# Kernel tuning notes

Measured on AMD Instinct MI355X. Metric: run time of the kernel, lower is better.

Reference implementation:

```python
import jax, jax.numpy as jnp
import numpy as np

B, S, H, E, V, OOV = 64, 400, 512, 256, 50000, 100

def setup_inputs() -> dict:
    key = jax.random.key(0)
    ks = jax.random.split(key, 32)
    p = lambda i, shape: jax.random.normal(ks[i], shape, jnp.float32) * 0.02
    emb = p(0, (V, E)).at[0].set(0.0)  # padding_idx=0
    return dict(
        summaries_in=jax.random.randint(ks[1], (B,), 1, V),
        h0=jax.random.normal(ks[2], (B, H), jnp.float32),
        c0=jax.random.normal(ks[3], (B, H), jnp.float32),
        encoder_out=jax.random.normal(ks[4], (B, S, 2 * H), jnp.float32),
        encoder_features=jax.random.normal(ks[5], (S * B, 2 * H), jnp.float32),
        encoder_mask=jnp.ones((S, B), jnp.float32),
        context=jax.random.normal(ks[6], (B, 2 * H), jnp.float32),
        coverage=jax.random.uniform(ks[7], (S, B), jnp.float32) * 0.01,
        texts_extended=jax.random.randint(ks[8], (S, B), 0, V + OOV),
        oov_size=OOV,
        emb=emb,
        W_feat=p(10, (2 * H, 2 * H)), b_feat=p(11, (2 * H,)),
        W_cov=p(12, (2 * H,)), b_cov=p(13, (2 * H,)),
        w_att=p(14, (2 * H,)), b_att=p(15, ()),
        W_ih=p(16, (4 * H, E)), W_hh=p(17, (4 * H, H)),
        b_ih=p(18, (4 * H,)), b_hh=p(19, (4 * H,)),
        W_ctx=p(20, (E, 2 * H + E)), b_ctx=p(21, (E,)),
        W_pg=p(22, (4 * H + E,)), b_pg=p(23, ()),
        W_o1=p(24, (H, 3 * H)), b_o1=p(25, (H,)),
        W_o2=p(26, (V, H)), b_o2=p(27, (V,)),
    )


def reference(summaries_in, h0, c0, encoder_out, encoder_features, encoder_mask,
              context, coverage, texts_extended, oov_size, emb,
              W_feat, b_feat, W_cov, b_cov, w_att, b_att,
              W_ih, W_hh, b_ih, b_hh, W_ctx, b_ctx, W_pg, b_pg,
              W_o1, b_o1, W_o2, b_o2):
    # embedding + context projection: [B, 2H+E] -> [B, E]
    x = emb[summaries_in]
    ctx_out = jnp.concatenate([context, x], axis=1) @ W_ctx.T + b_ctx
    # single LSTM step (torch gate order i, f, g, o)
    gates = ctx_out @ W_ih.T + b_ih + h0 @ W_hh.T + b_hh
    i, f, g, o = jnp.split(gates, 4, axis=1)
    c = jax.nn.sigmoid(f) * c0 + jax.nn.sigmoid(i) * jnp.tanh(g)
    h = jax.nn.sigmoid(o) * jnp.tanh(c)
    hidden_out = jnp.concatenate([h, c], axis=1)  # [B, 2H]
    # Bahdanau attention with coverage
    dec_feat = hidden_out @ W_feat.T + b_feat                 # [B, 2H]
    ef = encoder_features.reshape(S, B, 2 * H)                # [S, B, 2H]
    cov_feat = coverage[..., None] * W_cov + b_cov            # Linear(1, 2H)
    e = jnp.tanh(ef + dec_feat[None] + cov_feat) @ w_att + b_att  # [S, B]
    a = jax.nn.softmax(e, axis=0) * encoder_mask
    a = a / jnp.sum(a, axis=0, keepdims=True)                 # renormalize (Normalize(0))
    ctx_new = jnp.einsum('sb,bsd->bd', a, encoder_out)        # [B, 2H]
    coverage_next = coverage + a
    # pointer-generator mix
    gen_in = jnp.concatenate([ctx_new, hidden_out, ctx_out], axis=1)  # [B, 4H+E]
    p_gen = jax.nn.sigmoid(gen_in @ W_pg + b_pg)[:, None]             # [B, 1]
    logits = (jnp.concatenate([h, ctx_new], axis=1) @ W_o1.T + b_o1) @ W_o2.T + b_o2
    vocab_dist = p_gen * jax.nn.softmax(logits, axis=1)       # [B, V]
    attn_w = (1.0 - p_gen) * a.T                              # [B, S]
    vd = jnp.concatenate([vocab_dist, jnp.zeros((B, oov_size), vocab_dist.dtype)], axis=1)
    vd = vd.at[jnp.arange(B)[:, None], texts_extended.T].add(attn_w)  # scatter_add copy dist
    return vd, hidden_out, ctx_new, a, coverage_next
```

## Files before the change

kernel.cpp:

```cpp
#include <hip/hip_runtime.h>
#include <cmath>

#define B 64
#define S 400
#define H 512
#define E 256
#define V 50000
#define OOV 100
#define H2 1024
#define VDN (V + OOV)
#define NBLK_V 782
#define SC 10

typedef __attribute__((ext_vector_type(8))) short short8;
typedef __attribute__((ext_vector_type(4))) float f32x4;

__device__ __forceinline__ float wred_sum(float v) {
#pragma unroll
  for (int o = 32; o > 0; o >>= 1) v += __shfl_down(v, o, 64);
  return v;
}
__device__ __forceinline__ short f2bf(float f) {
  return __builtin_bit_cast(short, (__bf16)f);
}
__device__ __forceinline__ float bf2f(unsigned short u) {
  unsigned x = (unsigned)u << 16;
  return __builtin_bit_cast(float, x);
}
__device__ __forceinline__ float ftanh(float x) {
  float e = __expf(2.f * x);
  return 1.f - 2.f * __builtin_amdgcn_rcpf(e + 1.f);
}
__device__ __forceinline__ float fsig(float x) {
  return __builtin_amdgcn_rcpf(1.f + __expf(-x));
}
__device__ __forceinline__ float wred_max(float v) {
#pragma unroll
  for (int o = 32; o > 0; o >>= 1) v = fmaxf(v, __shfl_down(v, o, 64));
  return v;
}

__global__ __launch_bounds__(256) void k_pre(
    const float* __restrict__ b_ctx, const float* __restrict__ b_ih,
    const float* __restrict__ b_hh, const float* __restrict__ b_feat,
    const float* __restrict__ b_o1, const float* __restrict__ context,
    const float* __restrict__ emb, const int* __restrict__ sumin,
    const float* __restrict__ h0, float* __restrict__ ctxoutT4,
    float* __restrict__ gates, float* __restrict__ dfeat,
    float* __restrict__ innerT4, float* __restrict__ catT4,
    float* __restrict__ h0T4, float* __restrict__ Zb) {
  int idx = blockIdx.x * 256 + threadIdx.x;
  if (idx < 64) Zb[idx] = 0.f;
  if (idx < 16384) {
    int j = ((idx >> 8) << 2) + (idx & 3);
    ctxoutT4[idx] = b_ctx[j];
  } else if (idx < 16384 + 131072) {
    int i = idx - 16384;
    int j = i & 2047;
    gates[i] = b_ih[j] + b_hh[j];
  } else if (idx < 16384 + 131072 + 65536) {
    int i = idx - 16384 - 131072;
    dfeat[i] = b_feat[i & 1023];
  } else if (idx < 245760) {
    int i = idx - 16384 - 131072 - 65536;
    int j = ((i >> 8) << 2) + (i & 3);
    innerT4[i] = b_o1[j];
  } else if (idx < 245760 + 81920) {
    int i = idx - 245760;
    int e = i & 3, b = (i >> 2) & 63, q = i >> 8;
    int k = q * 4 + e;
    catT4[i] = (k < 1024) ? context[b * 1024 + k]
                          : emb[(size_t)sumin[b] * 256 + (k - 1024)];
  } else {
    int i = idx - 245760 - 81920;
    int e = i & 3, b = (i >> 2) & 63, q = i >> 8;
    h0T4[i] = h0[b * 512 + q * 4 + e];
  }
}

template <int R, int KC, int OUTMODE>
__global__ __launch_bounds__(256) void k_gemmsk(
    const float* __restrict__ A1, const float* __restrict__ W1, int ldw1, int s1,
    const float* __restrict__ A2, const float* __restrict__ W2, int ldw2,
    float* __restrict__ out, int ldout) {
  const int lane = threadIdx.x;
  const int w = threadIdx.y;
  const int j0 = blockIdx.x * (4 * R) + w * R;
  const float* A;
  const float* W;
  int ldw, kc0;
  if ((int)blockIdx.y < s1) {
    A = A1; W = W1; ldw = ldw1; kc0 = blockIdx.y * KC;
  } else {
    A = A2; W = W2; ldw = ldw2; kc0 = (blockIdx.y - s1) * KC;
  }
  float acc[R];
#pragma unroll
  for (int r = 0; r < R; ++r) acc[r] = 0.f;
  const float* ap = A + (size_t)kc0 * 256 + lane * 4;
  const float* wr[R];
#pragma unroll
  for (int r = 0; r < R; ++r) wr[r] = W + (size_t)(j0 + r) * ldw + kc0 * 4;
#pragma unroll 8
  for (int k4 = 0; k4 < KC; ++k4) {
    float4 av = *(const float4*)(ap + (size_t)k4 * 256);
#pragma unroll
    for (int r = 0; r < R; ++r) {
      float4 wv = *(const float4*)(wr[r] + k4 * 4);
      acc[r] += av.x * wv.x + av.y * wv.y + av.z * wv.z + av.w * wv.w;
    }
  }
#pragma unroll
  for (int r = 0; r < R; ++r) {
    int j = j0 + r;
    if constexpr (OUTMODE == 0)
      atomicAdd(&out[((size_t)(j >> 2) * 64 + lane) * 4 + (j & 3)], acc[r]);
    else
      atomicAdd(&out[(size_t)lane * ldout + j], acc[r]);
  }
}

__global__ __launch_bounds__(256) void k_lstm(const float* __restrict__ gates,
                                              const float* __restrict__ c0,
                                              float* __restrict__ hidden,
                                              float* __restrict__ hcT4) {
  int idx = blockIdx.x * 256 + threadIdx.x;
  int b = idx >> 9, u = idx & 511;
  float gi = gates[(size_t)b * 2048 + u];
  float gf = gates[(size_t)b * 2048 + 512 + u];
  float gg = gates[(size_t)b * 2048 + 1024 + u];
  float go = gates[(size_t)b * 2048 + 1536 + u];
  float c = fsig(gf) * c0[(size_t)b * 512 + u] + fsig(gi) * ftanh(gg);
  float h = fsig(go) * ftanh(c);
  hidden[(size_t)b * H2 + u] = h;
  hidden[(size_t)b * H2 + 512 + u] = c;
  hcT4[((u >> 2) * 64 + b) * 4 + (u & 3)] = h;
  int k = 512 + u;
  hcT4[((k >> 2) * 64 + b) * 4 + (k & 3)] = c;
}

__global__ __launch_bounds__(256) void k_ectx(
    const float* __restrict__ ef, const float* __restrict__ dfeat,
    const float* __restrict__ cov, const float* __restrict__ Wcov,
    const float* __restrict__ bcov, const float* __restrict__ watt,
    const float* __restrict__ batt, const float* __restrict__ mask,
    const float* __restrict__ enc, float* __restrict__ e_x,
    float* __restrict__ Zb, float* __restrict__ partc) {
  const int t = threadIdx.x;
  const int lane = t & 63;
  const int w = t >> 6;
  const int b = blockIdx.x & 63;
  const int g = blockIdx.x >> 6;
  const int s0 = g * 40 + w * 10;
  float4 dbc[4], wc4[4], wa4[4];
  {
    const float4* dfr = (const float4*)(dfeat + (size_t)b * H2);
    const float4* bcr = (const float4*)bcov;
    const float4* wcr = (const float4*)Wcov;
    const float4* war = (const float4*)watt;
#pragma unroll
    for (int k = 0; k < 4; ++k) {
      int i4 = k * 64 + lane;
      float4 dv = dfr[i4], bc = bcr[i4];
      dbc[k] = make_float4(dv.x + bc.x, dv.y + bc.y, dv.z + bc.z, dv.w + bc.w);
      wc4[k] = wcr[i4];
      wa4[k] = war[i4];
    }
  }
  const float ba = batt[0];
  float4 acc[4];
#pragma unroll
  for (int k = 0; k < 4; ++k) acc[k] = make_float4(0.f, 0.f, 0.f, 0.f);
  float zsum = 0.f;

  for (int i = 0; i < 10; i += 2) {
    const int s1 = s0 + i, s2 = s0 + i + 1;
    const float4* efr1 = (const float4*)(ef + (size_t)(s1 * B + b) * H2);
    const float4* efr2 = (const float4*)(ef + (size_t)(s2 * B + b) * H2);
    const float4* enr1 = (const float4*)(enc + ((size_t)b * S + s1) * H2);
    const float4* enr2 = (const float4*)(enc + ((size_t)b * S + s2) * H2);
    float4 a1[4], a2[4], e1[4], e2[4];
#pragma unroll
    for (int k = 0; k < 4; ++k) {
      int i4 = k * 64 + lane;
      a1[k] = efr1[i4];
      a2[k] = efr2[i4];
      e1[k] = enr1[i4];
      e2[k] = enr2[i4];
    }
    const float c1 = cov[s1 * B + b], c2 = cov[s2 * B + b];
    float d1 = 0.f, d2 = 0.f;
#pragma unroll
    for (int k = 0; k < 4; ++k) {
      d1 += ftanh(a1[k].x + dbc[k].x + c1 * wc4[k].x) * wa4[k].x;
      d1 += ftanh(a1[k].y + dbc[k].y + c1 * wc4[k].y) * wa4[k].y;
      d1 += ftanh(a1[k].z + dbc[k].z + c1 * wc4[k].z) * wa4[k].z;
      d1 += ftanh(a1[k].w + dbc[k].w + c1 * wc4[k].w) * wa4[k].w;
      d2 += ftanh(a2[k].x + dbc[k].x + c2 * wc4[k].x) * wa4[k].x;
      d2 += ftanh(a2[k].y + dbc[k].y + c2 * wc4[k].y) * wa4[k].y;
      d2 += ftanh(a2[k].z + dbc[k].z + c2 * wc4[k].z) * wa4[k].z;
      d2 += ftanh(a2[k].w + dbc[k].w + c2 * wc4[k].w) * wa4[k].w;
    }
#pragma unroll
    for (int o = 32; o > 0; o >>= 1) {
      d1 += __shfl_xor(d1, o, 64);
      d2 += __shfl_xor(d2, o, 64);
    }
    const float x1 = mask[s1 * B + b] * __expf(d1 + ba);
    const float x2 = mask[s2 * B + b] * __expf(d2 + ba);
    if (lane == 0) {
      e_x[s1 * B + b] = x1;
      e_x[s2 * B + b] = x2;
    }
    zsum += x1 + x2;
#pragma unroll
    for (int k = 0; k < 4; ++k) {
      acc[k].x += x1 * e1[k].x + x2 * e2[k].x;
      acc[k].y += x1 * e1[k].y + x2 * e2[k].y;
      acc[k].z += x1 * e1[k].z + x2 * e2[k].z;
      acc[k].w += x1 * e1[k].w + x2 * e2[k].w;
    }
  }
  if (lane == 0) atomicAdd(&Zb[b], zsum);
  __shared__ float4 lacc[4][256];
#pragma unroll
  for (int k = 0; k < 4; ++k) lacc[w][lane * 4 + k] = acc[k];
  __syncthreads();
  if (w == 0) {
#pragma unroll
    for (int k = 0; k < 4; ++k) {
      float4 s = lacc[0][lane * 4 + k];
      float4 s1 = lacc[1][lane * 4 + k];
      float4 s2 = lacc[2][lane * 4 + k];
      float4 s3 = lacc[3][lane * 4 + k];
      s.x += s1.x + s2.x + s3.x;
      s.y += s1.y + s2.y + s3.y;
      s.z += s1.z + s2.z + s3.z;
      s.w += s1.w + s2.w + s3.w;
      ((float4*)(partc + (size_t)blockIdx.x * H2))[k * 64 + lane] = s;
    }
  }
}

__global__ __launch_bounds__(256) void k_ctxpg(
    const float* __restrict__ partc, const float* __restrict__ e_x,
    const float* __restrict__ Zb, const float* __restrict__ coverage,
    const float* __restrict__ hidden, const float* __restrict__ ctxoutT4,
    const float* __restrict__ Wpg, const float* __restrict__ bpg,
    float* __restrict__ ctx_new, float* __restrict__ ctxT4,
    float* __restrict__ pgen, float* __restrict__ a_out,
    float* __restrict__ cov_out) {
  const int b = blockIdx.x;
  const int t = threadIdx.x;
  const int lane = t & 63, w = t >> 6;
  const float rZ = 1.f / Zb[b];
  const int d = t * 4;
  float4 s = make_float4(0.f, 0.f, 0.f, 0.f);
#pragma unroll
  for (int sc = 0; sc < SC; ++sc) {
    float4 v = *(const float4*)(partc + (size_t)(sc * 64 + b) * H2 + d);
    s.x += v.x; s.y += v.y; s.z += v.z; s.w += v.w;
  }
  s.x *= rZ; s.y *= rZ; s.z *= rZ; s.w *= rZ;
  *(float4*)(ctx_new + (size_t)b * H2 + d) = s;
  *(float4*)(ctxT4 + (size_t)t * 256 + b * 4) = s;
#pragma unroll
  for (int i = 0; i < 2; ++i) {
    int sidx = t + i * 256;
    if (sidx < S) {
      int sb = sidx * B + b;
      float av = e_x[sb] * rZ;
      a_out[sb] = av;
      cov_out[sb] = coverage[sb] + av;
    }
  }
  float p = s.x * Wpg[d] + s.y * Wpg[d + 1] + s.z * Wpg[d + 2] + s.w * Wpg[d + 3];
#pragma unroll
  for (int j = 0; j < 4; ++j) {
    int k = t + j * 256;
    p += hidden[(size_t)b * H2 + k] * Wpg[1024 + k];
  }
  p += ctxoutT4[(size_t)(t >> 2) * 256 + b * 4 + (t & 3)] * Wpg[2048 + t];
  p = wred_sum(p);
  __shared__ float red[4];
  if (lane == 0) red[w] = p;
  __syncthreads();
  if (t == 0) {
    float dd = red[0] + red[1] + red[2] + red[3] + bpg[0];
    pgen[b] = fsig(dd);
  }
}

__global__ __launch_bounds__(256) void k_packinner(const float* __restrict__ innerT4,
                                                   short8* __restrict__ packB) {
  int f = blockIdx.x * 256 + threadIdx.x;
  int l = f & 63, bt = (f >> 6) & 3, ks = f >> 8;
  int b = bt * 16 + (l & 15);
  int kbase = ks * 32 + (l >> 4) * 8;
  float4 q0 = *(const float4*)&innerT4[(size_t)(kbase / 4) * 256 + b * 4];
  float4 q1 = *(const float4*)&innerT4[(size_t)(kbase / 4 + 1) * 256 + b * 4];
  short8 frag;
  frag[0] = f2bf(q0.x); frag[1] = f2bf(q0.y);
  frag[2] = f2bf(q0.z); frag[3] = f2bf(q0.w);
  frag[4] = f2bf(q1.x); frag[5] = f2bf(q1.y);
  frag[6] = f2bf(q1.z); frag[7] = f2bf(q1.w);
  packB[f] = frag;
}

__global__ __launch_bounds__(256) void k_mfma_logits(
    const float* __restrict__ W2, const short8* __restrict__ packB,
    const float* __restrict__ bias, unsigned short* __restrict__ logits_bf,
    float* __restrict__ mp, float* __restrict__ zp) {
  const int l = threadIdx.x;
  const int w = threadIdx.y;
  const int jblk = blockIdx.x * 64;
  const int jv = min(jblk + w * 16 + (l & 15), V - 1);
  const float4* wp4 = (const float4*)(W2 + (size_t)jv * 512 + (l >> 4) * 8);

  f32x4 acc0 = {0.f, 0.f, 0.f, 0.f}, acc1 = acc0, acc2 = acc0, acc3 = acc0;
  float4 cw0 = wp4[0], cw1 = wp4[1];
#pragma unroll
  for (int ks = 0; ks < 16; ++ks) {
    float4 nw0, nw1;
    if (ks < 15) { nw0 = wp4[(ks + 1) * 8]; nw1 = wp4[(ks + 1) * 8 + 1]; }
    short8 af;
    af[0] = f2bf(cw0.x); af[1] = f2bf(cw0.y); af[2] = f2bf(cw0.z); af[3] = f2bf(cw0.w);
    af[4] = f2bf(cw1.x); af[5] = f2bf(cw1.y); af[6] = f2bf(cw1.z); af[7] = f2bf(cw1.w);
    short8 b0 = packB[(ks * 4 + 0) * 64 + l];
    short8 b1 = packB[(ks * 4 + 1) * 64 + l];
    short8 b2 = packB[(ks * 4 + 2) * 64 + l];
    short8 b3 = packB[(ks * 4 + 3) * 64 + l];
    acc0 = __builtin_amdgcn_mfma_f32_16x16x32_bf16(af, b0, acc0, 0, 0, 0);
    acc1 = __builtin_amdgcn_mfma_f32_16x16x32_bf16(af, b1, acc1, 0, 0, 0);
    acc2 = __builtin_amdgcn_mfma_f32_16x16x32_bf16(af, b2, acc2, 0, 0, 0);
    acc3 = __builtin_amdgcn_mfma_f32_16x16x32_bf16(af, b3, acc3, 0, 0, 0);
    if (ks < 15) { cw0 = nw0; cw1 = nw1; }
  }

  __shared__ float tile[64][65];
  const int rbase = w * 16 + (l >> 4) * 4;
#pragma unroll
  for (int v = 0; v < 4; ++v) {
    int jl = rbase + v;
    int j = jblk + jl;
    float bv = bias[min(j, V - 1)];
    bool valid = (j < V);
    tile[jl][0 * 16 + (l & 15)] = valid ? acc0[v] + bv : -INFINITY;
    tile[jl][1 * 16 + (l & 15)] = valid ? acc1[v] + bv : -INFINITY;
    tile[jl][2 * 16 + (l & 15)] = valid ? acc2[v] + bv : -INFINITY;
    tile[jl][3 * 16 + (l & 15)] = valid ? acc3[v] + bv : -INFINITY;
  }
  __syncthreads();
  const int t = w * 64 + l;
#pragma unroll
  for (int i = 0; i < 16; ++i) {
    int idx = i * 256 + t;
    int jl = idx & 63;
    int b = idx >> 6;
    int j = jblk + jl;
    if (j < V)
      logits_bf[(size_t)b * V + j] = (unsigned short)f2bf(tile[jl][b]);
  }
  if (t < 64) {
    float m = -INFINITY;
#pragma unroll
    for (int jl = 0; jl < 64; ++jl) m = fmaxf(m, tile[jl][t]);
    float z = 0.f;
#pragma unroll
    for (int jl = 0; jl < 64; ++jl) z += __expf(tile[jl][t] - m);
    mp[(size_t)blockIdx.x * 64 + t] = m;
    zp[(size_t)blockIdx.x * 64 + t] = z;
  }
}

__global__ __launch_bounds__(256) void k_vdms(
    const unsigned short* __restrict__ logits_bf, const float* __restrict__ mp,
    const float* __restrict__ zp, const float* __restrict__ pgen,
    const float* __restrict__ a_out, const int* __restrict__ tex,
    float* __restrict__ out) {
  const int b = blockIdx.x >> 3;
  const int c = blockIdx.x & 7;
  const int t = threadIdx.x;
  const int lane = t & 63, w = t >> 6;
  __shared__ float red[4];
  __shared__ float hist[6272];
  float m = -INFINITY;
  for (int i = t; i < NBLK_V; i += 256) m = fmaxf(m, mp[i * 64 + b]);
  m = wred_max(m);
  if (lane == 0) red[w] = m;
  __syncthreads();
  const float M = fmaxf(fmaxf(red[0], red[1]), fmaxf(red[2], red[3]));
  __syncthreads();
  float z = 0.f;
  for (int i = t; i < NBLK_V; i += 256) z += zp[i * 64 + b] * __expf(mp[i * 64 + b] - M);
  z = wred_sum(z);
  if (lane == 0) red[w] = z;
  __syncthreads();
  const float Z = red[0] + red[1] + red[2] + red[3];
  const float pg = pgen[b];
  const float scale = pg / Z;
  const float wq = 1.f - pg;
  const int v0 = c * 6272;
  const int v1 = min(v0 + 6272, VDN);
  for (int i = t; i < 6272; i += 256) hist[i] = 0.f;
  __syncthreads();
  for (int s = t; s < S; s += 256) {
    int v = tex[s * B + b];
    if (v >= v0 && v < v1) atomicAdd(&hist[v - v0], wq * a_out[s * B + b]);
  }
  __syncthreads();
  for (int v = v0 + t; v < v1; v += 256) {
    float val =
        (v < V) ? scale * __expf(bf2f(logits_bf[(size_t)b * V + v]) - M) : 0.f;
    out[(size_t)b * VDN + v] = val + hist[v - v0];
  }
}

extern "C" void kernel_launch(void* const* d_in, const int* in_sizes, int n_in,
                              void* d_out, int out_size, void* d_ws, size_t ws_size,
                              hipStream_t stream) {
  const int* sumin = (const int*)d_in[0];
  const float* h0 = (const float*)d_in[1];
  const float* c0 = (const float*)d_in[2];
  const float* enc_out = (const float*)d_in[3];
  const float* ef = (const float*)d_in[4];
  const float* mask = (const float*)d_in[5];
  const float* context = (const float*)d_in[6];
  const float* coverage = (const float*)d_in[7];
  const int* tex = (const int*)d_in[8];
  const float* emb = (const float*)d_in[10];
  const float* W_feat = (const float*)d_in[11];
  const float* b_feat = (const float*)d_in[12];
  const float* W_cov = (const float*)d_in[13];
  const float* b_cov = (const float*)d_in[14];
  const float* w_att = (const float*)d_in[15];
  const float* b_att = (const float*)d_in[16];
  const float* W_ih = (const float*)d_in[17];
  const float* W_hh = (const float*)d_in[18];
  const float* b_ih = (const float*)d_in[19];
  const float* b_hh = (const float*)d_in[20];
  const float* W_ctx = (const float*)d_in[21];
  const float* b_ctx = (const float*)d_in[22];
  const float* W_pg = (const float*)d_in[23];
  const float* b_pg = (const float*)d_in[24];
  const float* W_o1 = (const float*)d_in[25];
  const float* b_o1 = (const float*)d_in[26];
  const float* W_o2 = (const float*)d_in[27];
  const float* b_o2 = (const float*)d_in[28];

  float* out = (float*)d_out;
  float* vd = out;
  float* hidden = vd + (size_t)B * VDN;
  float* ctx_new = hidden + (size_t)B * H2;
  float* a_out = ctx_new + (size_t)B * H2;
  float* cov_out = a_out + (size_t)S * B;

  float* ws = (float*)d_ws;
  float* catT4 = ws;
  float* h0T4 = catT4 + 81920;
  float* ctxoutT4 = h0T4 + 32768;
  float* gates = ctxoutT4 + 16384;
  float* hidcatT4 = gates + 131072;
  float* dfeat = hidcatT4 + 65536;
  float* e_x = dfeat + 65536;
  float* ctxnewT4 = e_x + 25600;
  float* innerT4 = ctxnewT4 + 65536;
  float* pgen = innerT4 + 32768;
  float* Zb = pgen + 64;
  float* mp = Zb + 64;
  float* zp = mp + 50048;
  float* packBf = zp + 50048;
  float* logits = packBf + 16384;
  float* partc = logits + 1600064;
  short8* packB = (short8*)packBf;
  unsigned short* logits_bf = (unsigned short*)logits;

  dim3 gblk(64, 4);

  k_pre<<<1408, 256, 0, stream>>>(b_ctx, b_ih, b_hh, b_feat, b_o1, context, emb,
                                  sumin, h0, ctxoutT4, gates, dfeat, innerT4,
                                  catT4, h0T4, Zb);
  k_gemmsk<2, 64, 0><<<dim3(32, 5), gblk, 0, stream>>>(
      catT4, W_ctx, 1280, 5, nullptr, nullptr, 0, ctxoutT4, 0);
  k_gemmsk<2, 64, 1><<<dim3(256, 3), gblk, 0, stream>>>(
      ctxoutT4, W_ih, 256, 1, h0T4, W_hh, 512, gates, 2048);
  k_lstm<<<128, 256, 0, stream>>>(gates, c0, hidden, hidcatT4);
  k_gemmsk<2, 64, 1><<<dim3(128, 4), gblk, 0, stream>>>(
      hidcatT4, W_feat, 1024, 4, nullptr, nullptr, 0, dfeat, 1024);
  k_ectx<<<SC * B, 256, 0, stream>>>(ef, dfeat, coverage, W_cov, b_cov, w_att,
                                     b_att, mask, enc_out, e_x, Zb, partc);
  k_ctxpg<<<B, 256, 0, stream>>>(partc, e_x, Zb, coverage, hidden, ctxoutT4,
                                 W_pg, b_pg, ctx_new, ctxnewT4, pgen, a_out,
                                 cov_out);
  k_gemmsk<2, 64, 0><<<dim3(64, 6), gblk, 0, stream>>>(
      hidcatT4, W_o1, 1536, 2, ctxnewT4, W_o1 + 512, 1536, innerT4, 0);
  k_packinner<<<16, 256, 0, stream>>>(innerT4, packB);
  k_mfma_logits<<<NBLK_V, gblk, 0, stream>>>(W_o2, packB, b_o2, logits_bf, mp, zp);
  k_vdms<<<B * 8, 256, 0, stream>>>(logits_bf, mp, zp, pgen, a_out, tex, vd);
}
```

Baseline: 204.9 us.

## Restructure attention-context kernel for more blocks and upfront loads

The attention energy/context kernel now gives each warp 4 sequence positions instead of 10, so the grid grows from 10 to 25 position groups (SC raised to match). All encoder-feature and encoder-output rows for a warp are loaded into registers up front, behind a scheduling barrier, to expose more memory-level parallelism. Per-batch decoder-feature, coverage and attention weights are staged in shared memory, and the cross-warp reduction of partial contexts is done by all threads. In exchange there is higher register pressure, more partial-context rows for the downstream kernel to reduce, and more atomics on the normaliser.

```diff
diff --git a/kernel.cpp b/kernel.cpp
--- a/kernel.cpp
+++ b/kernel.cpp
@@ -10,7 +10,7 @@
 #define H2 1024
 #define VDN (V + OOV)
 #define NBLK_V 782
-#define SC 10
+#define SC 25
 
 typedef __attribute__((ext_vector_type(8))) short short8;
 typedef __attribute__((ext_vector_type(4))) float f32x4;
@@ -18,6 +18,11 @@
 __device__ __forceinline__ float wred_sum(float v) {
 #pragma unroll
   for (int o = 32; o > 0; o >>= 1) v += __shfl_down(v, o, 64);
+  return v;
+}
+__device__ __forceinline__ float wred_max(float v) {
+#pragma unroll
+  for (int o = 32; o > 0; o >>= 1) v = fmaxf(v, __shfl_down(v, o, 64));
   return v;
 }
 __device__ __forceinline__ short f2bf(float f) {
@@ -33,11 +38,6 @@
 }
 __device__ __forceinline__ float fsig(float x) {
   return __builtin_amdgcn_rcpf(1.f + __expf(-x));
-}
-__device__ __forceinline__ float wred_max(float v) {
-#pragma unroll
-  for (int o = 32; o > 0; o >>= 1) v = fmaxf(v, __shfl_down(v, o, 64));
-  return v;
 }
 
 __global__ __launch_bounds__(256) void k_pre(
@@ -151,94 +151,82 @@
   const int w = t >> 6;
   const int b = blockIdx.x & 63;
   const int g = blockIdx.x >> 6;
-  const int s0 = g * 40 + w * 10;
-  float4 dbc[4], wc4[4], wa4[4];
-  {
-    const float4* dfr = (const float4*)(dfeat + (size_t)b * H2);
-    const float4* bcr = (const float4*)bcov;
-    const float4* wcr = (const float4*)Wcov;
-    const float4* war = (const float4*)watt;
+  const int s0 = g * 16 + w * 4;
+  __shared__ float s_dbc[1024], s_wc[1024], s_wa[1024];
+  for (int i = t; i < 1024; i += 256) {
+    s_dbc[i] = dfeat[(size_t)b * H2 + i] + bcov[i];
+    s_wc[i] = Wcov[i];
+    s_wa[i] = watt[i];
+  }
+  __syncthreads();
+
+  float4 evs[4][4], ens[4][4];
+  float cv[4], mk[4];
+#pragma unroll
+  for (int r = 0; r < 4; ++r) {
+    const int s = s0 + r;
+    const float4* efr = (const float4*)(ef + (size_t)(s * B + b) * H2);
+    const float4* enr = (const float4*)(enc + ((size_t)b * S + s) * H2);
 #pragma unroll
     for (int k = 0; k < 4; ++k) {
-      int i4 = k * 64 + lane;
-      float4 dv = dfr[i4], bc = bcr[i4];
-      dbc[k] = make_float4(dv.x + bc.x, dv.y + bc.y, dv.z + bc.z, dv.w + bc.w);
-      wc4[k] = wcr[i4];
-      wa4[k] = war[i4];
+      evs[r][k] = efr[k * 64 + lane];
+      ens[r][k] = enr[k * 64 + lane];
     }
-  }
+    cv[r] = cov[s * B + b];
+    mk[r] = mask[s * B + b];
+  }
+  __builtin_amdgcn_sched_barrier(0);
+
   const float ba = batt[0];
+  float x[4];
+  float zsum = 0.f;
+#pragma unroll
+  for (int r = 0; r < 4; ++r) {
+    float d = 0.f;
+#pragma unroll
+    for (int k = 0; k < 4; ++k) {
+      const int i4 = (k * 64 + lane) * 4;
+      d += ftanh(evs[r][k].x + s_dbc[i4 + 0] + cv[r] * s_wc[i4 + 0]) * s_wa[i4 + 0];
+      d += ftanh(evs[r][k].y + s_dbc[i4 + 1] + cv[r] * s_wc[i4 + 1]) * s_wa[i4 + 1];
+      d += ftanh(evs[r][k].z + s_dbc[i4 + 2] + cv[r] * s_wc[i4 + 2]) * s_wa[i4 + 2];
+      d += ftanh(evs[r][k].w + s_dbc[i4 + 3] + cv[r] * s_wc[i4 + 3]) * s_wa[i4 + 3];
+    }
+#pragma unroll
+    for (int o = 32; o > 0; o >>= 1) d += __shfl_xor(d, o, 64);
+    x[r] = mk[r] * __expf(d + ba);
+    if (lane == 0) e_x[(s0 + r) * B + b] = x[r];
+    zsum += x[r];
+  }
+  if (lane == 0) atomicAdd(&Zb[b], zsum);
   float4 acc[4];
 #pragma unroll
   for (int k = 0; k < 4; ++k) acc[k] = make_float4(0.f, 0.f, 0.f, 0.f);
-  float zsum = 0.f;
-
-  for (int i = 0; i < 10; i += 2) {
-    const int s1 = s0 + i, s2 = s0 + i + 1;
-    const float4* efr1 = (const float4*)(ef + (size_t)(s1 * B + b) * H2);
-    const float4* efr2 = (const float4*)(ef + (size_t)(s2 * B + b) * H2);
-    const float4* enr1 = (const float4*)(enc + ((size_t)b * S + s1) * H2);
-    const float4* enr2 = (const float4*)(enc + ((size_t)b * S + s2) * H2);
-    float4 a1[4], a2[4], e1[4], e2[4];
+#pragma unroll
+  for (int r = 0; r < 4; ++r) {
 #pragma unroll
     for (int k = 0; k < 4; ++k) {
-      int i4 = k * 64 + lane;
-      a1[k] = efr1[i4];
-      a2[k] = efr2[i4];
-      e1[k] = enr1[i4];
-      e2[k] = enr2[i4];
+      acc[k].x += x[r] * ens[r][k].x;
+      acc[k].y += x[r] * ens[r][k].y;
+      acc[k].z += x[r] * ens[r][k].z;
+      acc[k].w += x[r] * ens[r][k].w;
     }
-    const float c1 = cov[s1 * B + b], c2 = cov[s2 * B + b];
-    float d1 = 0.f, d2 = 0.f;
-#pragma unroll
-    for (int k = 0; k < 4; ++k) {
-      d1 += ftanh(a1[k].x + dbc[k].x + c1 * wc4[k].x) * wa4[k].x;
-      d1 += ftanh(a1[k].y + dbc[k].y + c1 * wc4[k].y) * wa4[k].y;
-      d1 += ftanh(a1[k].z + dbc[k].z + c1 * wc4[k].z) * wa4[k].z;
-      d1 += ftanh(a1[k].w + dbc[k].w + c1 * wc4[k].w) * wa4[k].w;
-      d2 += ftanh(a2[k].x + dbc[k].x + c2 * wc4[k].x) * wa4[k].x;
-      d2 += ftanh(a2[k].y + dbc[k].y + c2 * wc4[k].y) * wa4[k].y;
-      d2 += ftanh(a2[k].z + dbc[k].z + c2 * wc4[k].z) * wa4[k].z;
-      d2 += ftanh(a2[k].w + dbc[k].w + c2 * wc4[k].w) * wa4[k].w;
-    }
-#pragma unroll
-    for (int o = 32; o > 0; o >>= 1) {
-      d1 += __shfl_xor(d1, o, 64);
-      d2 += __shfl_xor(d2, o, 64);
-    }
-    const float x1 = mask[s1 * B + b] * __expf(d1 + ba);
-    const float x2 = mask[s2 * B + b] * __expf(d2 + ba);
-    if (lane == 0) {
-      e_x[s1 * B + b] = x1;
-      e_x[s2 * B + b] = x2;
-    }
-    zsum += x1 + x2;
-#pragma unroll
-    for (int k = 0; k < 4; ++k) {
-      acc[k].x += x1 * e1[k].x + x2 * e2[k].x;
-      acc[k].y += x1 * e1[k].y + x2 * e2[k].y;
-      acc[k].z += x1 * e1[k].z + x2 * e2[k].z;
-      acc[k].w += x1 * e1[k].w + x2 * e2[k].w;
-    }
-  }
-  if (lane == 0) atomicAdd(&Zb[b], zsum);
-  __shared__ float4 lacc[4][256];
-#pragma unroll
-  for (int k = 0; k < 4; ++k) lacc[w][lane * 4 + k] = acc[k];
-  __syncthreads();
-  if (w == 0) {
-#pragma unroll
-    for (int k = 0; k < 4; ++k) {
-      float4 s = lacc[0][lane * 4 + k];
-      float4 s1 = lacc[1][lane * 4 + k];
-      float4 s2 = lacc[2][lane * 4 + k];
-      float4 s3 = lacc[3][lane * 4 + k];
-      s.x += s1.x + s2.x + s3.x;
-      s.y += s1.y + s2.y + s3.y;
-      s.z += s1.z + s2.z + s3.z;
-      s.w += s1.w + s2.w + s3.w;
-      ((float4*)(partc + (size_t)blockIdx.x * H2))[k * 64 + lane] = s;
-    }
+  }
+  __shared__ float lacc[4][16][64];
+#pragma unroll
+  for (int k = 0; k < 4; ++k) {
+    lacc[w][k * 4 + 0][lane] = acc[k].x;
+    lacc[w][k * 4 + 1][lane] = acc[k].y;
+    lacc[w][k * 4 + 2][lane] = acc[k].z;
+    lacc[w][k * 4 + 3][lane] = acc[k].w;
+  }
+  __syncthreads();
+#pragma unroll
+  for (int j = 0; j < 4; ++j) {
+    int dim = j * 256 + t;
+    int ln = (dim & 255) >> 2, c = dim & 3;
+    float ssum = lacc[0][j * 4 + c][ln] + lacc[1][j * 4 + c][ln] +
+                 lacc[2][j * 4 + c][ln] + lacc[3][j * 4 + c][ln];
+    partc[(size_t)blockIdx.x * H2 + dim] = ssum;
   }
 }
 
```

Measured after the change: 218.9 us. 1.07x slower.
